# Optimization experiments

Hardware: AMD Instinct MI355X
Metric: run time of the kernel (lower is better)

## Reference

```python
import jax, jax.numpy as jnp
import numpy as np

DIM = 768
HEADS = 12
HEAD_DIM = DIM // HEADS
B, N = 8, 512
LN_EPS = 1e-5


def setup_inputs() -> dict:
    key = jax.random.key(0)
    ks = jax.random.split(key, 6)
    x = jax.random.normal(ks[0], (B, N, DIM), dtype=jnp.float32)
    qkv_w = jax.random.normal(ks[1], (3 * DIM, DIM), dtype=jnp.float32) * (DIM ** -0.5)
    ln_w = jnp.ones((HEADS, N, N), dtype=jnp.float32)
    ln_b = jnp.zeros((HEADS, N, N), dtype=jnp.float32)
    proj_w = jax.random.normal(ks[2], (DIM, DIM), dtype=jnp.float32) * (DIM ** -0.5)
    proj_b = jnp.zeros((DIM,), dtype=jnp.float32)
    return {"x": x, "qkv_w": qkv_w, "ln_w": ln_w, "ln_b": ln_b,
            "proj_w": proj_w, "proj_b": proj_b}


def _grassmannian(t):
    # project each head vector onto the unit sphere (L2 normalize over head_dim)
    nrm = jnp.linalg.norm(t, axis=-1, keepdims=True)
    return t / nrm


def reference(x, qkv_w, ln_w, ln_b, proj_w, proj_b):
    b, n, c = x.shape
    qkv = (x @ qkv_w.T).reshape(b, n, 3, HEADS, HEAD_DIM)
    qkv = jnp.transpose(qkv, (2, 0, 3, 1, 4))  # (3, B, H, N, d)
    q, k, v = qkv[0], qkv[1], qkv[2]
    q = _grassmannian(q)
    k = _grassmannian(k)
    # ||outer(q_n, k_m)||_2^2 over head_dim == sum_d q_d^2 k_d^2 = (q^2) @ (k^2)^T
    attn = jnp.einsum('bhnd,bhmd->bhnm', q * q, k * k)  # (B, H, N, N)
    # LayerNorm over normalized_shape=(H, N, N), i.e. per batch element
    mean = jnp.mean(attn, axis=(1, 2, 3), keepdims=True)
    var = jnp.var(attn, axis=(1, 2, 3), keepdims=True)
    attn = (attn - mean) * jax.lax.rsqrt(var + LN_EPS) * ln_w + ln_b
    out = jnp.einsum('bhnm,bhmd->bhnd', attn, v)  # (B, H, N, d)
    out = jnp.transpose(out, (0, 2, 1, 3)).reshape(b, n, c)
    out = out @ proj_w.T + proj_b
    return out, attn
```

## Files before the change

### kernel.cpp

```cpp
#include <hip/hip_runtime.h>

typedef __attribute__((ext_vector_type(8))) short bf16x8;
typedef __attribute__((ext_vector_type(4))) float f32x4;

#define HEADS 12
#define NN 512
#define BB 8
#define DIM 768
#define LDK 72
#define LDV 136
#define OUT0_ELEMS ((size_t)BB*NN*DIM)

__device__ __forceinline__ ushort f2bf(float f) {
  union { float f; uint u; } v; v.f = f;
  uint r = v.u + 0x7fffu + ((v.u >> 16) & 1u);
  return (ushort)(r >> 16);
}

__global__ __launch_bounds__(256) void cvt3_kernel(
    const float* __restrict__ a, ushort* __restrict__ oa, int na8,
    const float* __restrict__ b, ushort* __restrict__ ob, int nb8,
    const float* __restrict__ c, ushort* __restrict__ oc, int nc8) {
  int i = blockIdx.x * 256 + threadIdx.x;
  const float* in; ushort* out;
  if (i < na8) { in = a; out = oa; }
  else if (i < na8 + nb8) { i -= na8; in = b; out = ob; }
  else { i -= na8 + nb8; if (i >= nc8) return; in = c; out = oc; }
  float4 x = ((const float4*)in)[i*2], y = ((const float4*)in)[i*2+1];
  uint4 o;
  o.x = f2bf(x.x) | ((uint)f2bf(x.y) << 16);
  o.y = f2bf(x.z) | ((uint)f2bf(x.w) << 16);
  o.z = f2bf(y.x) | ((uint)f2bf(y.y) << 16);
  o.w = f2bf(y.z) | ((uint)f2bf(y.w) << 16);
  ((uint4*)out)[i] = o;
}

__global__ __launch_bounds__(256) void qkv_gemm(
    const ushort* __restrict__ xb, const ushort* __restrict__ wb,
    ushort* __restrict__ q2b, ushort* __restrict__ k2b, ushort* __restrict__ vt)
{
  __shared__ ushort As[128 * LDK];
  __shared__ ushort Bs[128 * LDK];
  const int t = threadIdx.x, l = t & 63, w = t >> 6;
  const int bx = blockIdx.x, by = blockIdx.y;
  const int rowbase = by * 128, colbase = bx * 128;
  const int wr = w >> 1, wc = w & 1, lr = l & 15, lg = l >> 4;
  f32x4 acc[4][4] = {};

  for (int kc = 0; kc < DIM; kc += 64) {
    #pragma unroll
    for (int i = 0; i < 4; ++i) {
      int c = t + 256 * i;
      int r = c >> 3, k16 = c & 7;
      *(uint4*)(As + r * LDK + k16 * 8) =
          *(const uint4*)(xb + (size_t)(rowbase + r) * DIM + kc + k16 * 8);
      *(uint4*)(Bs + r * LDK + k16 * 8) =
          *(const uint4*)(wb + (size_t)(colbase + r) * DIM + kc + k16 * 8);
    }
    __syncthreads();
    #pragma unroll
    for (int ks = 0; ks < 2; ++ks) {
      bf16x8 af[4], bg[4];
      #pragma unroll
      for (int i = 0; i < 4; ++i)
        af[i] = *(const bf16x8*)(As + (wr*64 + i*16 + lr) * LDK + ks*32 + lg*8);
      #pragma unroll
      for (int j = 0; j < 4; ++j)
        bg[j] = *(const bf16x8*)(Bs + (wc*64 + j*16 + lr) * LDK + ks*32 + lg*8);
      #pragma unroll
      for (int i = 0; i < 4; ++i)
        #pragma unroll
        for (int j = 0; j < 4; ++j)
          acc[i][j] = __builtin_amdgcn_mfma_f32_16x16x32_bf16(af[i], bg[j], acc[i][j], 0, 0, 0);
    }
    __syncthreads();
  }

  const int gcol = colbase + wc * 64;
  const int sel = gcol / DIM;
  const int h = (gcol % DIM) / 64;
  if (sel < 2) {
    ushort* dst = (sel == 0) ? q2b : k2b;
    #pragma unroll
    for (int i = 0; i < 4; ++i) {
      #pragma unroll
      for (int r = 0; r < 4; ++r) {
        float vj[4]; float s = 0.f;
        #pragma unroll
        for (int j = 0; j < 4; ++j) { vj[j] = acc[i][j][r]; s += vj[j] * vj[j]; }
        #pragma unroll
        for (int off = 1; off < 16; off <<= 1) s += __shfl_xor(s, off);
        float inv = 1.0f / s;
        int row = rowbase + wr*64 + i*16 + lg*4 + r;
        int b = row >> 9, n = row & 511;
        ushort* o = dst + (((size_t)(b * HEADS + h) * NN + n) << 6);
        #pragma unroll
        for (int j = 0; j < 4; ++j) o[j*16 + lr] = f2bf(vj[j] * vj[j] * inv);
      }
    }
  } else {
    #pragma unroll
    for (int i = 0; i < 4; ++i) {
      int row0 = rowbase + wr*64 + i*16 + lg*4;
      int b = row0 >> 9, n0 = row0 & 511;
      #pragma unroll
      for (int j = 0; j < 4; ++j) {
        int d = j*16 + lr;
        ushort4 pk;
        pk.x = f2bf(acc[i][j][0]); pk.y = f2bf(acc[i][j][1]);
        pk.z = f2bf(acc[i][j][2]); pk.w = f2bf(acc[i][j][3]);
        *(ushort4*)(vt + (((size_t)(b * HEADS + h) * 64 + d) << 9) + n0) = pk;
      }
    }
  }
}

__global__ __launch_bounds__(256) void stats_kernel(
    const ushort* __restrict__ q2b, const ushort* __restrict__ k2b,
    double* __restrict__ hsum)
{
  __shared__ ushort Qs[256 * LDK];
  __shared__ ushort Ks[128 * LDK];
  __shared__ float red[8];
  const int t = threadIdx.x, l = t & 63, w = t >> 6;
  const int rt = blockIdx.x, h = blockIdx.y, b = blockIdx.z;
  const size_t bh = (size_t)(b * HEADS + h);
  const int rowbase = rt * 256;
  const int lr = l & 15, lg = l >> 4;
  #pragma unroll
  for (int i = 0; i < 8; ++i) {
    int c = t + 256 * i;
    int r = c >> 3, k16 = c & 7;
    *(uint4*)(Qs + r * LDK + k16 * 8) =
        *(const uint4*)(q2b + (bh << 15) + ((size_t)(rowbase + r) << 6) + k16 * 8);
  }
  float s1 = 0.f, s2 = 0.f;
  for (int ct = 0; ct < 4; ++ct) {
    #pragma unroll
    for (int i = 0; i < 4; ++i) {
      int c = t + 256 * i;
      int r = c >> 3, k16 = c & 7;
      *(uint4*)(Ks + r * LDK + k16 * 8) =
          *(const uint4*)(k2b + (bh << 15) + ((size_t)(ct*128 + r) << 6) + k16 * 8);
    }
    __syncthreads();
    bf16x8 af[4][2];
    #pragma unroll
    for (int i = 0; i < 4; ++i)
      #pragma unroll
      for (int ks = 0; ks < 2; ++ks)
        af[i][ks] = *(const bf16x8*)(Qs + (w*64 + i*16 + lr) * LDK + ks*32 + lg*8);
    #pragma unroll
    for (int j = 0; j < 8; ++j) {
      bf16x8 b0 = *(const bf16x8*)(Ks + (j*16 + lr) * LDK + lg*8);
      bf16x8 b1 = *(const bf16x8*)(Ks + (j*16 + lr) * LDK + 32 + lg*8);
      #pragma unroll
      for (int i = 0; i < 4; ++i) {
        f32x4 a = {};
        a = __builtin_amdgcn_mfma_f32_16x16x32_bf16(af[i][0], b0, a, 0, 0, 0);
        a = __builtin_amdgcn_mfma_f32_16x16x32_bf16(af[i][1], b1, a, 0, 0, 0);
        #pragma unroll
        for (int r = 0; r < 4; ++r) { s1 += a[r]; s2 += a[r]*a[r]; }
      }
    }
    __syncthreads();
  }
  #pragma unroll
  for (int off = 1; off < 64; off <<= 1) { s1 += __shfl_xor(s1, off); s2 += __shfl_xor(s2, off); }
  if (l == 0) { red[w] = s1; red[4 + w] = s2; }
  __syncthreads();
  if (t == 0) {
    double d1 = (double)red[0] + red[1] + red[2] + red[3];
    double d2 = (double)red[4] + red[5] + red[6] + red[7];
    atomicAdd(&hsum[b * 2], d1);
    atomicAdd(&hsum[b * 2 + 1], d2);
  }
}

__global__ __launch_bounds__(256) void norm_pv(
    const ushort* __restrict__ q2b, const ushort* __restrict__ k2b,
    const ushort* __restrict__ vt,
    const float* __restrict__ lnw, const float* __restrict__ lnb,
    const double* __restrict__ hsum,
    float* __restrict__ attn, ushort* __restrict__ obh)
{
  __shared__ ushort Qs[64 * LDK];
  __shared__ ushort Ks[128 * LDK];
  __shared__ ushort Vs[64 * LDV];
  __shared__ ushort Pb[64 * 128];
  const int t = threadIdx.x, l = t & 63, w = t >> 6;
  const int rt = blockIdx.x, h = blockIdx.y, b = blockIdx.z;
  const size_t bh = (size_t)(b * HEADS + h);
  const int rowbase = rt * 64;
  const int lr = l & 15, lg = l >> 4;
  const double cnt = (double)HEADS * NN * NN;
  double mu = hsum[b * 2] / cnt;
  double var = hsum[b * 2 + 1] / cnt - mu * mu;
  const float mean = (float)mu;
  const float istd = (float)(1.0 / sqrt(var + 1e-5));

  #pragma unroll
  for (int i = 0; i < 2; ++i) {
    int c = t + 256 * i;
    int r = c >> 3, k16 = c & 7;
    *(uint4*)(Qs + r * LDK + k16 * 8) =
        *(const uint4*)(q2b + (bh << 15) + ((size_t)(rowbase + r) << 6) + k16 * 8);
  }
  __syncthreads();
  bf16x8 qf[4][2];
  #pragma unroll
  for (int j = 0; j < 4; ++j)
    #pragma unroll
    for (int ks = 0; ks < 2; ++ks)
      qf[j][ks] = *(const bf16x8*)(Qs + (j*16 + lr) * LDK + ks*32 + lg*8);

  f32x4 opv[4] = {};

  for (int ct = 0; ct < 4; ++ct) {
    #pragma unroll
    for (int i = 0; i < 4; ++i) {
      int c = t + 256 * i;
      int r = c >> 3, k16 = c & 7;
      *(uint4*)(Ks + r * LDK + k16 * 8) =
          *(const uint4*)(k2b + (bh << 15) + ((size_t)(ct*128 + r) << 6) + k16 * 8);
    }
    #pragma unroll
    for (int i = 0; i < 4; ++i) {
      int c = t + 256 * i;
      int r = c >> 4, k16 = c & 15;
      *(uint4*)(Vs + r * LDV + k16 * 8) =
          *(const uint4*)(vt + (bh << 15) + ((size_t)r << 9) + ct*128 + k16 * 8);
    }
    __syncthreads();
    #pragma unroll
    for (int i = 0; i < 2; ++i) {
      bf16x8 a0 = *(const bf16x8*)(Ks + (w*32 + i*16 + lr) * LDK + lg*8);
      bf16x8 a1 = *(const bf16x8*)(Ks + (w*32 + i*16 + lr) * LDK + 32 + lg*8);
      const int mloc = w*32 + i*16 + lg*4;
      const int m0 = ct*128 + mloc;
      const int cch = mloc >> 3;
      #pragma unroll
      for (int j = 0; j < 4; ++j) {
        f32x4 a = {};
        a = __builtin_amdgcn_mfma_f32_16x16x32_bf16(a0, qf[j][0], a, 0, 0, 0);
        a = __builtin_amdgcn_mfma_f32_16x16x32_bf16(a1, qf[j][1], a, 0, 0, 0);
        const int n = j*16 + lr;
        const size_t rowoff = ((size_t)h * NN + rowbase + n) * NN + m0;
        const float4 lw4 = *(const float4*)(lnw + rowoff);
        const float4 lb4 = *(const float4*)(lnb + rowoff);
        f32x4 v;
        v[0] = (a[0] - mean) * istd * lw4.x + lb4.x;
        v[1] = (a[1] - mean) * istd * lw4.y + lb4.y;
        v[2] = (a[2] - mean) * istd * lw4.z + lb4.z;
        v[3] = (a[3] - mean) * istd * lw4.w + lb4.w;
        __builtin_nontemporal_store(v,
            (f32x4*)(attn + ((bh << 9) + rowbase + n) * NN + m0));
        uint pk01, pk23;
        asm("v_cvt_pk_bf16_f32 %0, %1, %2" : "=v"(pk01) : "v"(v[0]), "v"(v[1]));
        asm("v_cvt_pk_bf16_f32 %0, %1, %2" : "=v"(pk23) : "v"(v[2]), "v"(v[3]));
        const int pch = (cch & 8) | ((cch & 7) ^ (n & 7));
        uint2 pk = { pk01, pk23 };
        *(uint2*)(Pb + n*128 + pch*8 + (lg & 1)*4) = pk;
      }
    }
    __syncthreads();
    #pragma unroll
    for (int ks = 0; ks < 4; ++ks) {
      const int cc = ks*4 + lg;
      const int nl = w*16 + lr;
      const int pch = (cc & 8) | ((cc & 7) ^ (nl & 7));
      bf16x8 ap = *(const bf16x8*)(Pb + nl*128 + pch*8);
      #pragma unroll
      for (int j = 0; j < 4; ++j) {
        bf16x8 bv = *(const bf16x8*)(Vs + (j*16 + lr) * LDV + ks*32 + lg*8);
        opv[j] = __builtin_amdgcn_mfma_f32_16x16x32_bf16(ap, bv, opv[j], 0, 0, 0);
      }
    }
    __syncthreads();
  }
  #pragma unroll
  for (int j = 0; j < 4; ++j) {
    int gc = h * 64 + j*16 + lr;
    #pragma unroll
    for (int r = 0; r < 4; ++r) {
      int gr = b * NN + rowbase + w*16 + lg*4 + r;
      obh[(size_t)gr * DIM + gc] = f2bf(opv[j][r]);
    }
  }
}

__global__ __launch_bounds__(256) void proj_gemm(
    const ushort* __restrict__ obh, const ushort* __restrict__ pwb,
    const float* __restrict__ pb, float* __restrict__ out)
{
  __shared__ ushort As[128 * LDK];
  __shared__ ushort Bs[128 * LDK];
  const int t = threadIdx.x, l = t & 63, w = t >> 6;
  const int bx = blockIdx.x, by = blockIdx.y;
  const int rowbase = by * 128, colbase = bx * 128;
  const int wr = w >> 1, wc = w & 1, lr = l & 15, lg = l >> 4;
  f32x4 acc[4][4] = {};
  for (int kc = 0; kc < DIM; kc += 64) {
    #pragma unroll
    for (int i = 0; i < 4; ++i) {
      int c = t + 256 * i;
      int r = c >> 3, k16 = c & 7;
      *(uint4*)(As + r * LDK + k16 * 8) =
          *(const uint4*)(obh + (size_t)(rowbase + r) * DIM + kc + k16 * 8);
      *(uint4*)(Bs + r * LDK + k16 * 8) =
          *(const uint4*)(pwb + (size_t)(colbase + r) * DIM + kc + k16 * 8);
    }
    __syncthreads();
    #pragma unroll
    for (int ks = 0; ks < 2; ++ks) {
      bf16x8 af[4], bg[4];
      #pragma unroll
      for (int i = 0; i < 4; ++i)
        af[i] = *(const bf16x8*)(As + (wr*64 + i*16 + lr) * LDK + ks*32 + lg*8);
      #pragma unroll
      for (int j = 0; j < 4; ++j)
        bg[j] = *(const bf16x8*)(Bs + (wc*64 + j*16 + lr) * LDK + ks*32 + lg*8);
      #pragma unroll
      for (int i = 0; i < 4; ++i)
        #pragma unroll
        for (int j = 0; j < 4; ++j)
          acc[i][j] = __builtin_amdgcn_mfma_f32_16x16x32_bf16(af[i], bg[j], acc[i][j], 0, 0, 0);
    }
    __syncthreads();
  }
  #pragma unroll
  for (int i = 0; i < 4; ++i) {
    #pragma unroll
    for (int r = 0; r < 4; ++r) {
      int row = rowbase + wr*64 + i*16 + lg*4 + r;
      #pragma unroll
      for (int j = 0; j < 4; ++j) {
        int col = colbase + wc*64 + j*16 + lr;
        out[(size_t)row * DIM + col] = acc[i][j][r] + pb[col];
      }
    }
  }
}

extern "C" void kernel_launch(void* const* d_in, const int* in_sizes, int n_in,
                              void* d_out, int out_size, void* d_ws, size_t ws_size,
                              hipStream_t stream) {
  const float* x      = (const float*)d_in[0];
  const float* qkv_w  = (const float*)d_in[1];
  const float* ln_w   = (const float*)d_in[2];
  const float* ln_b   = (const float*)d_in[3];
  const float* proj_w = (const float*)d_in[4];
  const float* proj_b = (const float*)d_in[5];
  float* out      = (float*)d_out;
  float* attn_out = out + OUT0_ELEMS;

  char* ws = (char*)d_ws;
  double* hsum = (double*)ws;
  ushort* wb   = (ushort*)(ws + 256);
  ushort* pwb  = wb  + (size_t)2304 * 768;
  ushort* xb   = pwb + (size_t)768 * 768;
  ushort* q2b  = xb  + (size_t)4096 * 768;
  ushort* k2b  = q2b + ((size_t)BB * HEADS * NN << 6);
  ushort* vt   = k2b + ((size_t)BB * HEADS * NN << 6);
  ushort* obh  = vt  + ((size_t)BB * HEADS * NN << 6);

  hipMemsetAsync(hsum, 0, 128, stream);
  cvt3_kernel<<<dim3(2688), 256, 0, stream>>>(qkv_w, wb, 221184,
                                              proj_w, pwb, 73728,
                                              x, xb, 393216);
  qkv_gemm    <<<dim3(18, 32),        256, 0, stream>>>(xb, wb, q2b, k2b, vt);
  stats_kernel<<<dim3(2, HEADS, BB),  256, 0, stream>>>(q2b, k2b, hsum);
  norm_pv     <<<dim3(8, HEADS, BB),  256, 0, stream>>>(q2b, k2b, vt, ln_w, ln_b, hsum,
                                                        attn_out, obh);
  proj_gemm   <<<dim3(6, 32),         256, 0, stream>>>(obh, pwb, proj_b, out);
}
```

Measured before the change: 263.7 us.

## Load Q/K/V fragments directly from global memory and shrink stats tiles

The attention kernels stop staging Q, K and V tiles in shared memory. Each lane now loads its MFMA operand fragments straight from global memory, which removes the LDS copies and most of the barriers. The stats kernel handles 64 rows per block instead of 256, giving four times as many blocks with less work each and no Q shared buffer. The cost is more uncoalesced global traffic and duplicated K/V reads across waves, which now depend on cache hits, plus more atomics in the stats pass.

```diff
diff --git a/kernel.cpp b/kernel.cpp
--- a/kernel.cpp
+++ b/kernel.cpp
@@ -8,7 +8,6 @@
 #define BB 8
 #define DIM 768
 #define LDK 72
-#define LDV 136
 #define OUT0_ELEMS ((size_t)BB*NN*DIM)
 
 __device__ __forceinline__ ushort f2bf(float f) {
@@ -119,21 +118,18 @@
     const ushort* __restrict__ q2b, const ushort* __restrict__ k2b,
     double* __restrict__ hsum)
 {
-  __shared__ ushort Qs[256 * LDK];
   __shared__ ushort Ks[128 * LDK];
   __shared__ float red[8];
   const int t = threadIdx.x, l = t & 63, w = t >> 6;
   const int rt = blockIdx.x, h = blockIdx.y, b = blockIdx.z;
   const size_t bh = (size_t)(b * HEADS + h);
-  const int rowbase = rt * 256;
+  const int rowbase = rt * 64;
   const int lr = l & 15, lg = l >> 4;
-  #pragma unroll
-  for (int i = 0; i < 8; ++i) {
-    int c = t + 256 * i;
-    int r = c >> 3, k16 = c & 7;
-    *(uint4*)(Qs + r * LDK + k16 * 8) =
-        *(const uint4*)(q2b + (bh << 15) + ((size_t)(rowbase + r) << 6) + k16 * 8);
-  }
+  bf16x8 af[2];
+  #pragma unroll
+  for (int ks = 0; ks < 2; ++ks)
+    af[ks] = *(const bf16x8*)(q2b + (bh << 15) +
+                              ((size_t)(rowbase + w*16 + lr) << 6) + ks*32 + lg*8);
   float s1 = 0.f, s2 = 0.f;
   for (int ct = 0; ct < 4; ++ct) {
     #pragma unroll
@@ -144,24 +140,15 @@
           *(const uint4*)(k2b + (bh << 15) + ((size_t)(ct*128 + r) << 6) + k16 * 8);
     }
     __syncthreads();
-    bf16x8 af[4][2];
-    #pragma unroll
-    for (int i = 0; i < 4; ++i)
-      #pragma unroll
-      for (int ks = 0; ks < 2; ++ks)
-        af[i][ks] = *(const bf16x8*)(Qs + (w*64 + i*16 + lr) * LDK + ks*32 + lg*8);
     #pragma unroll
     for (int j = 0; j < 8; ++j) {
       bf16x8 b0 = *(const bf16x8*)(Ks + (j*16 + lr) * LDK + lg*8);
       bf16x8 b1 = *(const bf16x8*)(Ks + (j*16 + lr) * LDK + 32 + lg*8);
-      #pragma unroll
-      for (int i = 0; i < 4; ++i) {
-        f32x4 a = {};
-        a = __builtin_amdgcn_mfma_f32_16x16x32_bf16(af[i][0], b0, a, 0, 0, 0);
-        a = __builtin_amdgcn_mfma_f32_16x16x32_bf16(af[i][1], b1, a, 0, 0, 0);
-        #pragma unroll
-        for (int r = 0; r < 4; ++r) { s1 += a[r]; s2 += a[r]*a[r]; }
-      }
+      f32x4 a = {};
+      a = __builtin_amdgcn_mfma_f32_16x16x32_bf16(af[0], b0, a, 0, 0, 0);
+      a = __builtin_amdgcn_mfma_f32_16x16x32_bf16(af[1], b1, a, 0, 0, 0);
+      #pragma unroll
+      for (int r = 0; r < 4; ++r) { s1 += a[r]; s2 += a[r]*a[r]; }
     }
     __syncthreads();
   }
@@ -184,9 +171,6 @@
     const double* __restrict__ hsum,
     float* __restrict__ attn, ushort* __restrict__ obh)
 {
-  __shared__ ushort Qs[64 * LDK];
-  __shared__ ushort Ks[128 * LDK];
-  __shared__ ushort Vs[64 * LDV];
   __shared__ ushort Pb[64 * 128];
   const int t = threadIdx.x, l = t & 63, w = t >> 6;
   const int rt = blockIdx.x, h = blockIdx.y, b = blockIdx.z;
@@ -199,43 +183,23 @@
   const float mean = (float)mu;
   const float istd = (float)(1.0 / sqrt(var + 1e-5));
 
-  #pragma unroll
-  for (int i = 0; i < 2; ++i) {
-    int c = t + 256 * i;
-    int r = c >> 3, k16 = c & 7;
-    *(uint4*)(Qs + r * LDK + k16 * 8) =
-        *(const uint4*)(q2b + (bh << 15) + ((size_t)(rowbase + r) << 6) + k16 * 8);
-  }
-  __syncthreads();
   bf16x8 qf[4][2];
   #pragma unroll
   for (int j = 0; j < 4; ++j)
     #pragma unroll
     for (int ks = 0; ks < 2; ++ks)
-      qf[j][ks] = *(const bf16x8*)(Qs + (j*16 + lr) * LDK + ks*32 + lg*8);
+      qf[j][ks] = *(const bf16x8*)(q2b + (bh << 15) +
+                    ((size_t)(rowbase + j*16 + lr) << 6) + ks*32 + lg*8);
 
   f32x4 opv[4] = {};
 
   for (int ct = 0; ct < 4; ++ct) {
     #pragma unroll
-    for (int i = 0; i < 4; ++i) {
-      int c = t + 256 * i;
-      int r = c >> 3, k16 = c & 7;
-      *(uint4*)(Ks + r * LDK + k16 * 8) =
-          *(const uint4*)(k2b + (bh << 15) + ((size_t)(ct*128 + r) << 6) + k16 * 8);
-    }
-    #pragma unroll
-    for (int i = 0; i < 4; ++i) {
-      int c = t + 256 * i;
-      int r = c >> 4, k16 = c & 15;
-      *(uint4*)(Vs + r * LDV + k16 * 8) =
-          *(const uint4*)(vt + (bh << 15) + ((size_t)r << 9) + ct*128 + k16 * 8);
-    }
-    __syncthreads();
-    #pragma unroll
     for (int i = 0; i < 2; ++i) {
-      bf16x8 a0 = *(const bf16x8*)(Ks + (w*32 + i*16 + lr) * LDK + lg*8);
-      bf16x8 a1 = *(const bf16x8*)(Ks + (w*32 + i*16 + lr) * LDK + 32 + lg*8);
+      const ushort* krow = k2b + (bh << 15) +
+                           ((size_t)(ct*128 + w*32 + i*16 + lr) << 6);
+      bf16x8 a0 = *(const bf16x8*)(krow + lg*8);
+      bf16x8 a1 = *(const bf16x8*)(krow + 32 + lg*8);
       const int mloc = w*32 + i*16 + lg*4;
       const int m0 = ct*128 + mloc;
       const int cch = mloc >> 3;
@@ -272,7 +236,8 @@
       bf16x8 ap = *(const bf16x8*)(Pb + nl*128 + pch*8);
       #pragma unroll
       for (int j = 0; j < 4; ++j) {
-        bf16x8 bv = *(const bf16x8*)(Vs + (j*16 + lr) * LDV + ks*32 + lg*8);
+        bf16x8 bv = *(const bf16x8*)(vt + (bh << 15) +
+                      ((size_t)(j*16 + lr) << 9) + ct*128 + ks*32 + lg*8);
         opv[j] = __builtin_amdgcn_mfma_f32_16x16x32_bf16(ap, bv, opv[j], 0, 0, 0);
       }
     }
@@ -369,7 +334,7 @@
                                               proj_w, pwb, 73728,
                                               x, xb, 393216);
   qkv_gemm    <<<dim3(18, 32),        256, 0, stream>>>(xb, wb, q2b, k2b, vt);
-  stats_kernel<<<dim3(2, HEADS, BB),  256, 0, stream>>>(q2b, k2b, hsum);
+  stats_kernel<<<dim3(8, HEADS, BB),  256, 0, stream>>>(q2b, k2b, hsum);
   norm_pv     <<<dim3(8, HEADS, BB),  256, 0, stream>>>(q2b, k2b, vt, ln_w, ln_b, hsum,
                                                         attn_out, obh);
   proj_gemm   <<<dim3(6, 32),         256, 0, stream>>>(obh, pwb, proj_b, out);
```

New measurement: 293.9 us. 11.4% more time.
